# Kernel tuning notes

Measured on AMD Instinct MI355X. Metric: run time of the kernel, lower is better.

The kernel has to match this reference:

```python
import jax, jax.numpy as jnp
import numpy as np

N_WIRES = 4
N_REUP = 3
N_Q_LAYERS = 2
SEQ_LEN = 10
GRU_HIDDEN = 16


def setup_inputs() -> dict:
    key = jax.random.key(0)
    ks = jax.random.split(key, 24)
    N, E = 10000, 320000
    s = 0.25
    inp = {
        'x': jax.random.normal(ks[0], (N, SEQ_LEN + 3), jnp.float32),
        'edge_index': jax.random.randint(ks[1], (2, E), 0, N, dtype=jnp.int32),
        'edge_attr': jax.random.normal(ks[2], (E, 1), jnp.float32),
        'W_ih': jax.random.normal(ks[3], (3 * GRU_HIDDEN, 1), jnp.float32) * s,
        'W_hh': jax.random.normal(ks[4], (3 * GRU_HIDDEN, GRU_HIDDEN), jnp.float32) * s,
        'b_ih': jax.random.normal(ks[5], (3 * GRU_HIDDEN,), jnp.float32) * s,
        'b_hh': jax.random.normal(ks[6], (3 * GRU_HIDDEN,), jnp.float32) * s,
        'p1_W': jax.random.normal(ks[7], (N_WIRES, GRU_HIDDEN + 3), jnp.float32) * s,
        'p1_b': jax.random.normal(ks[8], (N_WIRES,), jnp.float32) * s,
        'a1_W': jax.random.normal(ks[9], (1, 2 * N_WIRES), jnp.float32) * s,
        'q1_w': jax.random.uniform(ks[10], (N_REUP, N_Q_LAYERS, 2), jnp.float32, -np.pi, np.pi),
        'g1': jnp.ones((N_WIRES,), jnp.float32),
        'be1': jnp.zeros((N_WIRES,), jnp.float32),
        'p2_W': jax.random.normal(ks[11], (N_WIRES, N_WIRES), jnp.float32) * s,
        'p2_b': jax.random.normal(ks[12], (N_WIRES,), jnp.float32) * s,
        'a2_W': jax.random.normal(ks[13], (1, 2 * N_WIRES), jnp.float32) * s,
        'q2_w': jax.random.uniform(ks[14], (N_REUP, N_Q_LAYERS, 2), jnp.float32, -np.pi, np.pi),
        'g2': jnp.ones((N_WIRES,), jnp.float32),
        'be2': jnp.zeros((N_WIRES,), jnp.float32),
        'r_W': jax.random.normal(ks[15], (1, N_WIRES), jnp.float32) * s,
        'r_b': jax.random.normal(ks[16], (1,), jnp.float32) * s,
    }
    return inp


def _ry(theta):
    c = jnp.cos(theta * 0.5)
    s = jnp.sin(theta * 0.5)
    return jnp.stack([jnp.stack([c, -s], -1), jnp.stack([s, c], -1)], -2).astype(jnp.complex64)


def _rz(theta):
    em = jnp.exp(-0.5j * theta)
    ep = jnp.exp(0.5j * theta)
    z = jnp.zeros_like(em)
    return jnp.stack([jnp.stack([em, z], -1), jnp.stack([z, ep], -1)], -2)


def _apply1q(state, gate, wire):
    # state: [E,2,2,2,2]; gate: [2,2] shared or [E,2,2] per-edge
    st = jnp.moveaxis(state, 1 + wire, -1)
    if gate.ndim == 3:
        st = jnp.einsum('eij,e...j->e...i', gate, st)
    else:
        st = jnp.einsum('ij,e...j->e...i', gate, st)
    return jnp.moveaxis(st, -1, 1 + wire)


def _cnot(state, c, t):
    st = jnp.moveaxis(state, (1 + c, 1 + t), (-2, -1))
    st = jnp.concatenate([st[..., :1, :], st[..., 1:, ::-1]], axis=-2)
    return jnp.moveaxis(st, (-2, -1), (1 + c, 1 + t))


def _qcircuit(inputs, corr, weights):
    # inputs: [E,4] angles, corr: [E], weights: [3,2,2]; batched 4-wire statevector sim
    E = inputs.shape[0]
    state = jnp.zeros((E, 16), jnp.complex64).at[:, 0].set(1.0).reshape(E, 2, 2, 2, 2)
    for r in range(N_REUP):
        for i in range(N_WIRES):
            state = _apply1q(state, _ry(inputs[:, i]), i)
        state = _apply1q(state, _ry(corr), 0)
        for d in range(N_Q_LAYERS):
            gy = _ry(weights[r, d, 0])
            gz = _rz(weights[r, d, 1])
            for i in range(N_WIRES):
                state = _apply1q(state, gy, i)
                state = _apply1q(state, gz, i)
            for i in range(d % 2, N_WIRES - 1, 2):
                state = _cnot(state, i, i + 1)
    probs = state.real ** 2 + state.imag ** 2
    z = jnp.array([1.0, -1.0], jnp.float32)
    return jnp.stack(
        [jnp.einsum('e...j,j->e', jnp.moveaxis(probs, 1 + w, -1), z) for w in range(N_WIRES)], -1)


def _layernorm(x, g, b):
    mu = x.mean(-1, keepdims=True)
    v = ((x - mu) ** 2).mean(-1, keepdims=True)
    return (x - mu) * jax.lax.rsqrt(v + 1e-5) * g + b


def _qgat(x, edge_index, edge_attr, Wp, bp, Wa, qw, g, b):
    N = x.shape[0]
    h = jax.nn.elu(x @ Wp.T + bp)  # [N,4]
    sl = jnp.arange(N, dtype=edge_index.dtype)
    src = jnp.concatenate([edge_index[0], sl])
    dst = jnp.concatenate([edge_index[1], sl])
    ea = jnp.concatenate([edge_attr[:, 0], jnp.ones((N,), x.dtype)])
    alpha = jnp.concatenate([h[src], h[dst]], -1) @ Wa[0]  # [Et]
    alpha = jax.nn.leaky_relu(alpha, 0.2) * jnp.abs(ea)
    alpha = alpha - jax.lax.stop_gradient(alpha).max()
    aexp = jnp.exp(alpha)
    dsum = jax.ops.segment_sum(aexp, dst, num_segments=N)
    alpha = aexp / (dsum[dst] + 1e-8)
    corr = jnp.tanh(ea) * jnp.pi
    msg = alpha[:, None] * _qcircuit(jnp.tanh(h[src]) * jnp.pi, corr, qw)  # [Et,4]
    aggr = jax.ops.segment_sum(msg, dst, num_segments=N)
    return _layernorm(aggr + h, g, b)


def _gru_last(price_seq, W_ih, W_hh, b_ih, b_hh):
    # price_seq: [N,T] scalar-per-step GRU; returns final hidden [N,H]
    N = price_seq.shape[0]
    h0 = jnp.zeros((N, GRU_HIDDEN), price_seq.dtype)
    w_in = W_ih[:, 0]  # [3H]

    def step(h, x_t):
        gi = x_t[:, None] * w_in + b_ih  # [N,3H]
        gh = h @ W_hh.T + b_hh
        ir, iz, inn = jnp.split(gi, 3, -1)
        hr, hz, hn = jnp.split(gh, 3, -1)
        r = jax.nn.sigmoid(ir + hr)
        z = jax.nn.sigmoid(iz + hz)
        n = jnp.tanh(inn + r * hn)
        return (1.0 - z) * n + z * h, None

    h, _ = jax.lax.scan(step, h0, price_seq.T)
    return h


def reference(x, edge_index, edge_attr, W_ih, W_hh, b_ih, b_hh,
              p1_W, p1_b, a1_W, q1_w, g1, be1,
              p2_W, p2_b, a2_W, q2_w, g2, be2, r_W, r_b):
    hT = _gru_last(x[:, :SEQ_LEN], W_ih, W_hh, b_ih, b_hh)
    h = jnp.concatenate([hT, x[:, SEQ_LEN:]], -1)  # [N,19]
    h = jax.nn.relu(_qgat(h, edge_index, edge_attr, p1_W, p1_b, a1_W, q1_w, g1, be1))
    h = _qgat(h, edge_index, edge_attr, p2_W, p2_b, a2_W, q2_w, g2, be2)
    return (h @ r_W.T + r_b)[:, 0]
```

## Files before the change

kernel.cpp:

```cpp
#include <hip/hip_runtime.h>
#include <math.h>


#define GH 16
#define SEQ 10
#define PI_F 3.14159265358979323846f

__device__ __forceinline__ float sigmoidf_(float x) { return 1.0f / (1.0f + expf(-x)); }

__global__ __launch_bounds__(256) void k_gru(
    const float* __restrict__ x, const float* __restrict__ W_ih,
    const float* __restrict__ W_hh, const float* __restrict__ b_ih,
    const float* __restrict__ b_hh, const float* __restrict__ p1W,
    const float* __restrict__ p1b, const float* __restrict__ a1W,
    const float* __restrict__ q1w, const float* __restrict__ q2w,
    const int* __restrict__ ei, int* __restrict__ deg,
    float* __restrict__ nrec1, float* __restrict__ hdd1,
    float* __restrict__ qcs, int N, int E)
{
    for (int e = blockIdx.x * 256 + threadIdx.x; e < E; e += gridDim.x * 256)
        atomicAdd(&deg[ei[E + e]], 1);

    __shared__ float sW[48 * 16];
    __shared__ float sp1W[4 * 19], sp1b[4];
    for (int i = threadIdx.x; i < 48 * 16; i += 256) sW[i] = W_hh[i];
    if (threadIdx.x < 76) sp1W[threadIdx.x] = p1W[threadIdx.x];
    if (threadIdx.x < 4) sp1b[threadIdx.x] = p1b[threadIdx.x];
    __syncthreads();

    if (blockIdx.x == 0 && threadIdx.x < 12) {
        const float* qw = (threadIdx.x < 6) ? q1w : q2w;
        int rd = threadIdx.x % 6;
        float sy, cy; sincosf(0.5f * qw[rd * 2 + 0], &sy, &cy);
        float sz, cz; sincosf(0.5f * qw[rd * 2 + 1], &sz, &cz);
        float* q = qcs + threadIdx.x * 4;
        q[0] = cy; q[1] = sy; q[2] = cz; q[3] = sz;
    }

    const int j = threadIdx.x & 15;
    const int n = blockIdx.x * 16 + (threadIdx.x >> 4);
    const bool valid = (n < N);

    float wr[GH], wz[GH], wn[GH];
#pragma unroll
    for (int k = 0; k < GH; ++k) {
        wr[k] = sW[j * 16 + k];
        wz[k] = sW[(16 + j) * 16 + k];
        wn[k] = sW[(32 + j) * 16 + k];
    }
    float wir = W_ih[j], wiz = W_ih[16 + j], win_ = W_ih[32 + j];
    float bir = b_ih[j], biz = b_ih[16 + j], bin_ = b_ih[32 + j];
    float brr = b_hh[j], brz = b_hh[16 + j], brn = b_hh[32 + j];

    float xv[13];
#pragma unroll
    for (int t = 0; t < 13; ++t) xv[t] = valid ? x[n * 13 + t] : 0.f;

    float h = 0.f;
#pragma unroll
    for (int t = 0; t < SEQ; ++t) {
        float xt = xv[t];
        float ghr = brr, ghz = brz, ghn = brn;
#pragma unroll
        for (int k = 0; k < GH; ++k) {
            float hk = __shfl(h, k, 16);
            ghr += wr[k] * hk; ghz += wz[k] * hk; ghn += wn[k] * hk;
        }
        float r  = sigmoidf_(xt * wir + bir + ghr);
        float z  = sigmoidf_(xt * wiz + biz + ghz);
        float nv = tanhf(xt * win_ + bin_ + r * ghn);
        h = (1.f - z) * nv + z * h;
    }

    float s0 = h * sp1W[0 * 19 + j];
    float s1 = h * sp1W[1 * 19 + j];
    float s2 = h * sp1W[2 * 19 + j];
    float s3 = h * sp1W[3 * 19 + j];
#pragma unroll
    for (int m = 1; m < 16; m <<= 1) {
        s0 += __shfl_xor(s0, m, 16);
        s1 += __shfl_xor(s1, m, 16);
        s2 += __shfl_xor(s2, m, 16);
        s3 += __shfl_xor(s3, m, 16);
    }
    if (valid && j < 4) {
        float s = (j == 0) ? s0 : (j == 1) ? s1 : (j == 2) ? s2 : s3;
        s += sp1b[j] + xv[10] * sp1W[j * 19 + 16] + xv[11] * sp1W[j * 19 + 17]
           + xv[12] * sp1W[j * 19 + 18];
        float hv = (s > 0.f) ? s : expm1f(s);
        float* nb = nrec1 + (size_t)n * 16;
        float sv, cv; sincosf(0.5f * PI_F * tanhf(hv), &sv, &cv);
        nb[2 * j]     = cv;
        nb[2 * j + 1] = sv;
        nb[12 + j]    = hv;
        float ds = hv * a1W[j];
        float dd = hv * a1W[4 + j];
        ds += __shfl_xor(ds, 1); ds += __shfl_xor(ds, 2);
        dd += __shfl_xor(dd, 1); dd += __shfl_xor(dd, 2);
        if (j == 0) { nb[8] = ds; hdd1[n] = dd; }
    }
}

__global__ __launch_bounds__(256) void k_scan(
    const int* __restrict__ deg, int* __restrict__ off,
    int* __restrict__ cur, int N)
{
    __shared__ int part[256];
    const int t = threadIdx.x;
    const int chunk = (N + 255) / 256;
    const int lo = t * chunk;
    const int hi = min(lo + chunk, N);
    int s = 0;
    for (int i = lo; i < hi; ++i) s += deg[i] + 1;
    part[t] = s;
    __syncthreads();
    for (int d = 1; d < 256; d <<= 1) {
        int y = (t >= d) ? part[t - d] : 0;
        __syncthreads();
        part[t] += y;
        __syncthreads();
    }
    int run = part[t] - s;
    for (int i = lo; i < hi; ++i) { off[i] = run; cur[i] = run; run += deg[i] + 1; }
}

__global__ __launch_bounds__(256) void k_fill(
    const int* __restrict__ ei, const float* __restrict__ ea,
    int* __restrict__ cur, float2* __restrict__ rec,
    int* __restrict__ dstv, int E, int N)
{
    int idx = blockIdx.x * 256 + threadIdx.x;
    if (idx >= E + N) return;
    int src, d; float ev;
    if (idx < E) { src = ei[idx]; d = ei[E + idx]; ev = ea[idx]; }
    else         { src = idx - E; d = src;         ev = 1.0f;    }
    int slot = atomicAdd(&cur[d], 1);
    float2 r; r.x = __int_as_float(src); r.y = ev;
    rec[slot] = r;
    dstv[slot] = d;
}

template <int STR>
__device__ __forceinline__ void ry_g(float (&sr)[16], float (&si)[16], float c, float s) {
#pragma unroll
    for (int i0 = 0; i0 < 16; ++i0) {
        if (i0 & STR) continue;
        int i1 = i0 | STR;
        float a0r = sr[i0], a0i = si[i0], a1r = sr[i1], a1i = si[i1];
        sr[i0] = c * a0r - s * a1r; si[i0] = c * a0i - s * a1i;
        sr[i1] = s * a0r + c * a1r; si[i1] = s * a0i + c * a1i;
    }
}
template <int STR>
__device__ __forceinline__ void rz_g(float (&sr)[16], float (&si)[16], float c, float s) {
#pragma unroll
    for (int i = 0; i < 16; ++i) {
        float r = sr[i], im = si[i];
        if (i & STR) { sr[i] = r * c - im * s; si[i] = im * c + r * s; }
        else         { sr[i] = r * c + im * s; si[i] = im * c - r * s; }
    }
}
template <int SC, int ST>
__device__ __forceinline__ void cnot_g(float (&sr)[16], float (&si)[16]) {
#pragma unroll
    for (int i = 0; i < 16; ++i) {
        if ((i & SC) && !(i & ST)) {
            int j = i | ST;
            float tr = sr[i], ti = si[i];
            sr[i] = sr[j]; si[i] = si[j]; sr[j] = tr; si[j] = ti;
        }
    }
}

__device__ __forceinline__ void qcirc(
    float mc, float ms, float c1, float s1, float c2, float s2,
    float c3, float s3, const float* __restrict__ qc, float (&z)[4])
{
    float sr[16], si[16];
    float t0 = mc * c1, t1 = mc * s1, t2 = ms * c1, t3 = ms * s1;
    float u0 = c2 * c3, u1 = c2 * s3, u2 = s2 * c3, u3 = s2 * s3;
    sr[0]  = t0 * u0; sr[1]  = t0 * u1; sr[2]  = t0 * u2; sr[3]  = t0 * u3;
    sr[4]  = t1 * u0; sr[5]  = t1 * u1; sr[6]  = t1 * u2; sr[7]  = t1 * u3;
    sr[8]  = t2 * u0; sr[9]  = t2 * u1; sr[10] = t2 * u2; sr[11] = t2 * u3;
    sr[12] = t3 * u0; sr[13] = t3 * u1; sr[14] = t3 * u2; sr[15] = t3 * u3;
#pragma unroll
    for (int i = 0; i < 16; ++i) si[i] = 0.f;

#pragma unroll
    for (int r = 0; r < 3; ++r) {
        if (r > 0) {
            ry_g<8>(sr, si, mc, ms);
            ry_g<4>(sr, si, c1, s1);
            ry_g<2>(sr, si, c2, s2);
            ry_g<1>(sr, si, c3, s3);
        }
#pragma unroll
        for (int d = 0; d < 2; ++d) {
            const bool lastd = (r == 2 && d == 1);
            int rd = r * 2 + d;
            float cy = qc[rd * 4 + 0], sy = qc[rd * 4 + 1];
            float cz = qc[rd * 4 + 2], sz = qc[rd * 4 + 3];
            ry_g<8>(sr, si, cy, sy); if (!lastd) rz_g<8>(sr, si, cz, sz);
            ry_g<4>(sr, si, cy, sy); if (!lastd) rz_g<4>(sr, si, cz, sz);
            ry_g<2>(sr, si, cy, sy); if (!lastd) rz_g<2>(sr, si, cz, sz);
            ry_g<1>(sr, si, cy, sy); if (!lastd) rz_g<1>(sr, si, cz, sz);
            if (d == 0) { cnot_g<8, 4>(sr, si); cnot_g<2, 1>(sr, si); }
            else        { cnot_g<4, 2>(sr, si); }
        }
    }

    float p[16];
#pragma unroll
    for (int i = 0; i < 16; ++i) p[i] = sr[i] * sr[i] + si[i] * si[i];
#pragma unroll
    for (int w = 0; w < 4; ++w) {
        const int STR = 8 >> w;
        float zz = 0.f;
#pragma unroll
        for (int i = 0; i < 16; ++i) if (!(i & STR)) zz += p[i];
        z[w] = 2.f * zz - 1.f;
    }
}

__global__ __launch_bounds__(256) void k_edge(
    const float2* __restrict__ rec, const int* __restrict__ dstv,
    const float* __restrict__ nrec, const float* __restrict__ hdd,
    const float* __restrict__ qcsL, float* __restrict__ S, int EN)
{
    const int slot = blockIdx.x * 256 + threadIdx.x;
    const int lane = threadIdx.x & 63;
    const bool valid = slot < EN;
    int dst = -1;
    float a0 = 0.f, a1 = 0.f, a2 = 0.f, a3 = 0.f, a4 = 0.f;

    if (valid) {
        dst = dstv[slot];
        float2 r = rec[slot];
        int src = __float_as_int(r.x);
        float eav = r.y;
        const float* sb = nrec + (size_t)src * 16;
        float4 c01 = *reinterpret_cast<const float4*>(sb);
        float4 c23 = *reinterpret_cast<const float4*>(sb + 4);
        float s0 = sb[8] + hdd[dst];
        s0 = (s0 > 0.f) ? s0 : 0.2f * s0;
        float aexp = expf(s0 * fabsf(eav));

        float scv, ccv; sincosf(0.5f * PI_F * tanhf(eav), &scv, &ccv);
        float mc = c01.x * ccv - c01.y * scv;
        float ms = c01.y * ccv + c01.x * scv;

        float z[4];
        qcirc(mc, ms, c01.z, c01.w, c23.x, c23.y, c23.z, c23.w, qcsL, z);
        a0 = aexp * z[0]; a1 = aexp * z[1]; a2 = aexp * z[2]; a3 = aexp * z[3];
        a4 = aexp;
    }

    int prevd = __shfl_up(dst, 1);
    bool head = (lane == 0) || (prevd != dst);
    unsigned long long hm = __ballot(head);
    unsigned long long below = (2ull << lane) - 1ull;
    int H = 63 - __clzll((long long)(hm & below));
    int dist = lane - H;
#pragma unroll
    for (int st = 1; st < 64; st <<= 1) {
        float t0 = __shfl_up(a0, st), t1 = __shfl_up(a1, st),
              t2 = __shfl_up(a2, st), t3 = __shfl_up(a3, st),
              t4 = __shfl_up(a4, st);
        if (dist >= st) { a0 += t0; a1 += t1; a2 += t2; a3 += t3; a4 += t4; }
    }
    int nextd = __shfl_down(dst, 1);
    bool lastl = (lane == 63) || (dst != nextd);
    if (lastl && dst >= 0) {
        float* sbase = S + (size_t)dst * 5;
        atomicAdd(sbase + 0, a0); atomicAdd(sbase + 1, a1);
        atomicAdd(sbase + 2, a2); atomicAdd(sbase + 3, a3);
        atomicAdd(sbase + 4, a4);
    }
}

template <bool FINAL>
__global__ __launch_bounds__(256) void k_node(
    const float* __restrict__ S, const float* __restrict__ nrec,
    const float* __restrict__ g4, const float* __restrict__ be4,
    const float* __restrict__ pW, const float* __restrict__ pb,
    const float* __restrict__ WaN, const float* __restrict__ rW,
    const float* __restrict__ rb, float* __restrict__ onrec,
    float* __restrict__ ohdd, float* __restrict__ out, int N)
{
    int n = blockIdx.x * 256 + threadIdx.x;
    if (n >= N) return;
    const float* sb = S + (size_t)n * 5;
    const float* nb = nrec + (size_t)n * 16;
    float dn = sb[4] + 1e-8f;
    float v0 = sb[0] / dn + nb[12];
    float v1 = sb[1] / dn + nb[13];
    float v2 = sb[2] / dn + nb[14];
    float v3 = sb[3] / dn + nb[15];
    float mu = 0.25f * (v0 + v1 + v2 + v3);
    float d0 = v0 - mu, d1 = v1 - mu, d2 = v2 - mu, d3 = v3 - mu;
    float var = 0.25f * (d0 * d0 + d1 * d1 + d2 * d2 + d3 * d3);
    float rs = 1.0f / sqrtf(var + 1e-5f);
    float y0 = d0 * rs * g4[0] + be4[0];
    float y1 = d1 * rs * g4[1] + be4[1];
    float y2 = d2 * rs * g4[2] + be4[2];
    float y3 = d3 * rs * g4[3] + be4[3];

    if (FINAL) {
        out[n] = rb[0] + y0 * rW[0] + y1 * rW[1] + y2 * rW[2] + y3 * rW[3];
    } else {
        y0 = fmaxf(y0, 0.f); y1 = fmaxf(y1, 0.f);
        y2 = fmaxf(y2, 0.f); y3 = fmaxf(y3, 0.f);
        float hv[4];
#pragma unroll
        for (int w = 0; w < 4; ++w) {
            float s = pb[w] + y0 * pW[w * 4 + 0] + y1 * pW[w * 4 + 1]
                    + y2 * pW[w * 4 + 2] + y3 * pW[w * 4 + 3];
            hv[w] = (s > 0.f) ? s : expm1f(s);
        }
        float* ob = onrec + (size_t)n * 16;
        float ds = 0.f, dd = 0.f;
#pragma unroll
        for (int w = 0; w < 4; ++w) {
            float sv, cv; sincosf(0.5f * PI_F * tanhf(hv[w]), &sv, &cv);
            ob[2 * w]     = cv;
            ob[2 * w + 1] = sv;
            ob[12 + w]    = hv[w];
            ds += hv[w] * WaN[w];
            dd += hv[w] * WaN[4 + w];
        }
        ob[8] = ds;
        ohdd[n] = dd;
    }
}

extern "C" void kernel_launch(void* const* d_in, const int* in_sizes, int n_in,
                              void* d_out, int out_size, void* d_ws, size_t ws_size,
                              hipStream_t stream)
{
    const float* x    = (const float*)d_in[0];
    const int*   ei   = (const int*)d_in[1];
    const float* ea   = (const float*)d_in[2];
    const float* W_ih = (const float*)d_in[3];
    const float* W_hh = (const float*)d_in[4];
    const float* b_ih = (const float*)d_in[5];
    const float* b_hh = (const float*)d_in[6];
    const float* p1W  = (const float*)d_in[7];
    const float* p1b  = (const float*)d_in[8];
    const float* a1W  = (const float*)d_in[9];
    const float* q1w  = (const float*)d_in[10];
    const float* g1   = (const float*)d_in[11];
    const float* be1  = (const float*)d_in[12];
    const float* p2W  = (const float*)d_in[13];
    const float* p2b  = (const float*)d_in[14];
    const float* a2W  = (const float*)d_in[15];
    const float* q2w  = (const float*)d_in[16];
    const float* g2   = (const float*)d_in[17];
    const float* be2  = (const float*)d_in[18];
    const float* rW   = (const float*)d_in[19];
    const float* rb   = (const float*)d_in[20];
    float* out = (float*)d_out;

    int N  = in_sizes[0] / 13;
    int E  = in_sizes[1] / 2;
    int EN = E + N;

    float* ws    = (float*)d_ws;
    float* nrec1 = ws;
    float* nrec2 = nrec1 + (size_t)N * 16;
    float* hdd1  = nrec2 + (size_t)N * 16;
    float* hdd2  = hdd1 + N;
    float* qcs   = hdd2 + N;
    float* S1    = qcs + 64;
    float* S2    = S1 + (size_t)N * 5;
    int* deg  = (int*)(S2 + (size_t)N * 5);
    int* off  = deg + N;
    int* cur  = off + N;
    int* dstv = cur + N;
    uintptr_t rp = (uintptr_t)(dstv + EN);
    rp = (rp + 15u) & ~(uintptr_t)15u;
    float2* rec = (float2*)rp;

    hipMemsetAsync(S1, 0, ((size_t)N * 10 + N) * sizeof(float), stream);

    const int B = 256;
    k_gru<<<(N + 15) / 16, B, 0, stream>>>(x, W_ih, W_hh, b_ih, b_hh, p1W, p1b,
                                           a1W, q1w, q2w, ei, deg, nrec1, hdd1,
                                           qcs, N, E);
    k_scan<<<1, B, 0, stream>>>(deg, off, cur, N);
    k_fill<<<(EN + B - 1) / B, B, 0, stream>>>(ei, ea, cur, rec, dstv, E, N);

    k_edge<<<(EN + B - 1) / B, B, 0, stream>>>(rec, dstv, nrec1, hdd1, qcs, S1, EN);
    k_node<false><<<(N + B - 1) / B, B, 0, stream>>>(
        S1, nrec1, g1, be1, p2W, p2b, a2W, rW, rb, nrec2, hdd2, out, N);

    k_edge<<<(EN + B - 1) / B, B, 0, stream>>>(rec, dstv, nrec2, hdd2, qcs + 24, S2, EN);
    k_node<true><<<(N + B - 1) / B, B, 0, stream>>>(
        S2, nrec2, g2, be2, p2W, p2b, a2W, rW, rb, nrec2, hdd2, out, N);
}
```

Before: 265.2 us.

## Precompute edge rotation in fill, process two edges per thread, widen scan

The fill kernel now computes the edge-attribute rotation (sincos of tanh) once and stores it with src and dst in a float4 record, plus |ea| in a separate array, so both edge passes skip that math. Each edge-kernel thread handles two slots (g and g+G), issuing all gathers up front to raise memory-level parallelism, and runs two segmented reductions. The scan runs with 1024 threads, and zeroing of the S buffers moves into the GRU kernel so only deg is memset. The cost is a larger per-edge record to read and more registers per thread in the edge kernel.

```diff
diff --git a/kernel.cpp b/kernel.cpp
--- a/kernel.cpp
+++ b/kernel.cpp
@@ -16,8 +16,10 @@
     const float* __restrict__ q1w, const float* __restrict__ q2w,
     const int* __restrict__ ei, int* __restrict__ deg,
     float* __restrict__ nrec1, float* __restrict__ hdd1,
-    float* __restrict__ qcs, int N, int E)
-{
+    float* __restrict__ qcs, float* __restrict__ Sz, int N, int E)
+{
+    for (int i = blockIdx.x * 256 + threadIdx.x; i < N * 10; i += gridDim.x * 256)
+        Sz[i] = 0.f;
     for (int e = blockIdx.x * 256 + threadIdx.x; e < E; e += gridDim.x * 256)
         atomicAdd(&deg[ei[E + e]], 1);
 
@@ -101,20 +103,20 @@
     }
 }
 
-__global__ __launch_bounds__(256) void k_scan(
+__global__ __launch_bounds__(1024) void k_scan(
     const int* __restrict__ deg, int* __restrict__ off,
     int* __restrict__ cur, int N)
 {
-    __shared__ int part[256];
+    __shared__ int part[1024];
     const int t = threadIdx.x;
-    const int chunk = (N + 255) / 256;
+    const int chunk = (N + 1023) / 1024;
     const int lo = t * chunk;
     const int hi = min(lo + chunk, N);
     int s = 0;
     for (int i = lo; i < hi; ++i) s += deg[i] + 1;
     part[t] = s;
     __syncthreads();
-    for (int d = 1; d < 256; d <<= 1) {
+    for (int d = 1; d < 1024; d <<= 1) {
         int y = (t >= d) ? part[t - d] : 0;
         __syncthreads();
         part[t] += y;
@@ -126,8 +128,8 @@
 
 __global__ __launch_bounds__(256) void k_fill(
     const int* __restrict__ ei, const float* __restrict__ ea,
-    int* __restrict__ cur, float2* __restrict__ rec,
-    int* __restrict__ dstv, int E, int N)
+    int* __restrict__ cur, float4* __restrict__ rec,
+    float* __restrict__ aeav, int E, int N)
 {
     int idx = blockIdx.x * 256 + threadIdx.x;
     if (idx >= E + N) return;
@@ -135,9 +137,12 @@
     if (idx < E) { src = ei[idx]; d = ei[E + idx]; ev = ea[idx]; }
     else         { src = idx - E; d = src;         ev = 1.0f;    }
     int slot = atomicAdd(&cur[d], 1);
-    float2 r; r.x = __int_as_float(src); r.y = ev;
+    float scv, ccv; sincosf(0.5f * PI_F * tanhf(ev), &scv, &ccv);
+    float4 r;
+    r.x = __int_as_float(src); r.y = __int_as_float(d);
+    r.z = ccv; r.w = scv;
     rec[slot] = r;
-    dstv[slot] = d;
+    aeav[slot] = fabsf(ev);
 }
 
 template <int STR>
@@ -222,39 +227,10 @@
     }
 }
 
-__global__ __launch_bounds__(256) void k_edge(
-    const float2* __restrict__ rec, const int* __restrict__ dstv,
-    const float* __restrict__ nrec, const float* __restrict__ hdd,
-    const float* __restrict__ qcsL, float* __restrict__ S, int EN)
-{
-    const int slot = blockIdx.x * 256 + threadIdx.x;
-    const int lane = threadIdx.x & 63;
-    const bool valid = slot < EN;
-    int dst = -1;
-    float a0 = 0.f, a1 = 0.f, a2 = 0.f, a3 = 0.f, a4 = 0.f;
-
-    if (valid) {
-        dst = dstv[slot];
-        float2 r = rec[slot];
-        int src = __float_as_int(r.x);
-        float eav = r.y;
-        const float* sb = nrec + (size_t)src * 16;
-        float4 c01 = *reinterpret_cast<const float4*>(sb);
-        float4 c23 = *reinterpret_cast<const float4*>(sb + 4);
-        float s0 = sb[8] + hdd[dst];
-        s0 = (s0 > 0.f) ? s0 : 0.2f * s0;
-        float aexp = expf(s0 * fabsf(eav));
-
-        float scv, ccv; sincosf(0.5f * PI_F * tanhf(eav), &scv, &ccv);
-        float mc = c01.x * ccv - c01.y * scv;
-        float ms = c01.y * ccv + c01.x * scv;
-
-        float z[4];
-        qcirc(mc, ms, c01.z, c01.w, c23.x, c23.y, c23.z, c23.w, qcsL, z);
-        a0 = aexp * z[0]; a1 = aexp * z[1]; a2 = aexp * z[2]; a3 = aexp * z[3];
-        a4 = aexp;
-    }
-
+__device__ __forceinline__ void segreduce(
+    int dst, int lane, float a0, float a1, float a2, float a3, float a4,
+    float* __restrict__ S)
+{
     int prevd = __shfl_up(dst, 1);
     bool head = (lane == 0) || (prevd != dst);
     unsigned long long hm = __ballot(head);
@@ -276,6 +252,62 @@
         atomicAdd(sbase + 2, a2); atomicAdd(sbase + 3, a3);
         atomicAdd(sbase + 4, a4);
     }
+}
+
+__global__ __launch_bounds__(256) void k_edge(
+    const float4* __restrict__ rec, const float* __restrict__ aeav,
+    const float* __restrict__ nrec, const float* __restrict__ hdd,
+    const float* __restrict__ qcsL, float* __restrict__ S, int EN, int G)
+{
+    const int g = blockIdx.x * 256 + threadIdx.x;
+    const int lane = threadIdx.x & 63;
+    const int sA = g, sB = g + G;
+    const bool vA = sA < EN, vB = sB < EN;
+
+    float4 rA = vA ? rec[sA] : make_float4(0.f, 0.f, 1.f, 0.f);
+    float4 rB = vB ? rec[sB] : make_float4(0.f, 0.f, 1.f, 0.f);
+    float aeA = vA ? aeav[sA] : 0.f;
+    float aeB = vB ? aeav[sB] : 0.f;
+    int srcA = __float_as_int(rA.x), dstA = vA ? __float_as_int(rA.y) : -1;
+    int srcB = __float_as_int(rB.x), dstB = vB ? __float_as_int(rB.y) : -1;
+    const float* sbA = nrec + (size_t)(vA ? srcA : 0) * 16;
+    const float* sbB = nrec + (size_t)(vB ? srcB : 0) * 16;
+    float4 c01A = *reinterpret_cast<const float4*>(sbA);
+    float4 c23A = *reinterpret_cast<const float4*>(sbA + 4);
+    float hsA = sbA[8];
+    float hdA = hdd[vA ? dstA : 0];
+    float4 c01B = *reinterpret_cast<const float4*>(sbB);
+    float4 c23B = *reinterpret_cast<const float4*>(sbB + 4);
+    float hsB = sbB[8];
+    float hdB = hdd[vB ? dstB : 0];
+
+    float a0 = 0.f, a1 = 0.f, a2 = 0.f, a3 = 0.f, a4 = 0.f;
+    if (vA) {
+        float s0 = hsA + hdA;
+        s0 = (s0 > 0.f) ? s0 : 0.2f * s0;
+        float aexp = expf(s0 * aeA);
+        float mc = c01A.x * rA.z - c01A.y * rA.w;
+        float ms = c01A.y * rA.z + c01A.x * rA.w;
+        float z[4];
+        qcirc(mc, ms, c01A.z, c01A.w, c23A.x, c23A.y, c23A.z, c23A.w, qcsL, z);
+        a0 = aexp * z[0]; a1 = aexp * z[1]; a2 = aexp * z[2]; a3 = aexp * z[3];
+        a4 = aexp;
+    }
+    segreduce(dstA, lane, a0, a1, a2, a3, a4, S);
+
+    a0 = a1 = a2 = a3 = a4 = 0.f;
+    if (vB) {
+        float s0 = hsB + hdB;
+        s0 = (s0 > 0.f) ? s0 : 0.2f * s0;
+        float aexp = expf(s0 * aeB);
+        float mc = c01B.x * rB.z - c01B.y * rB.w;
+        float ms = c01B.y * rB.z + c01B.x * rB.w;
+        float z[4];
+        qcirc(mc, ms, c01B.z, c01B.w, c23B.x, c23B.y, c23B.z, c23B.w, qcsL, z);
+        a0 = aexp * z[0]; a1 = aexp * z[1]; a2 = aexp * z[2]; a3 = aexp * z[3];
+        a4 = aexp;
+    }
+    segreduce(dstB, lane, a0, a1, a2, a3, a4, S);
 }
 
 template <bool FINAL>
@@ -372,28 +404,32 @@
     float* qcs   = hdd2 + N;
     float* S1    = qcs + 64;
     float* S2    = S1 + (size_t)N * 5;
-    int* deg  = (int*)(S2 + (size_t)N * 5);
+    float* aeav  = S2 + (size_t)N * 5;
+    int* deg  = (int*)(aeav + EN);
     int* off  = deg + N;
     int* cur  = off + N;
-    int* dstv = cur + N;
-    uintptr_t rp = (uintptr_t)(dstv + EN);
+    uintptr_t rp = (uintptr_t)(cur + N);
     rp = (rp + 15u) & ~(uintptr_t)15u;
-    float2* rec = (float2*)rp;
-
-    hipMemsetAsync(S1, 0, ((size_t)N * 10 + N) * sizeof(float), stream);
+    float4* rec = (float4*)rp;
+
+    hipMemsetAsync(deg, 0, (size_t)N * sizeof(int), stream);
 
     const int B = 256;
     k_gru<<<(N + 15) / 16, B, 0, stream>>>(x, W_ih, W_hh, b_ih, b_hh, p1W, p1b,
                                            a1W, q1w, q2w, ei, deg, nrec1, hdd1,
-                                           qcs, N, E);
-    k_scan<<<1, B, 0, stream>>>(deg, off, cur, N);
-    k_fill<<<(EN + B - 1) / B, B, 0, stream>>>(ei, ea, cur, rec, dstv, E, N);
-
-    k_edge<<<(EN + B - 1) / B, B, 0, stream>>>(rec, dstv, nrec1, hdd1, qcs, S1, EN);
+                                           qcs, S1, N, E);
+    k_scan<<<1, 1024, 0, stream>>>(deg, off, cur, N);
+    k_fill<<<(EN + B - 1) / B, B, 0, stream>>>(ei, ea, cur, rec, aeav, E, N);
+
+    int half = (EN + 1) / 2;
+    int eblocks = (half + B - 1) / B;
+    int G = eblocks * B;
+
+    k_edge<<<eblocks, B, 0, stream>>>(rec, aeav, nrec1, hdd1, qcs, S1, EN, G);
     k_node<false><<<(N + B - 1) / B, B, 0, stream>>>(
         S1, nrec1, g1, be1, p2W, p2b, a2W, rW, rb, nrec2, hdd2, out, N);
 
-    k_edge<<<(EN + B - 1) / B, B, 0, stream>>>(rec, dstv, nrec2, hdd2, qcs + 24, S2, EN);
+    k_edge<<<eblocks, B, 0, stream>>>(rec, aeav, nrec2, hdd2, qcs + 24, S2, EN, G);
     k_node<true><<<(N + B - 1) / B, B, 0, stream>>>(
         S2, nrec2, g2, be2, p2W, p2b, a2W, rW, rb, nrec2, hdd2, out, N);
 }
```

Result: faster. 257.2 us (-3.0%).

## Precompute per-node quantum circuit moments so edge kernel evaluates a quadratic form

Applied to the files above, without the earlier changes.

The circuit's dependence on the edge is isolated to wire 0's rotation, so the per-node part of the circuit (fixed gate matrices plus the node's encoding) is folded into a per-node table of 40 quadratic coefficients. The edge kernel then only needs a degree-6 polynomial in cos/sin rather than simulating the 16-amplitude state for every edge. Edge-attribute trig is moved into the CSR fill, src/dst are packed into one word, the S zeroing moves into the GRU kernel, and the scan uses 1024 threads. The packing assumes node ids fit in 16 bits, and the per-node table adds an extra kernel and 48 floats of traffic per node.

```diff
diff --git a/kernel.cpp b/kernel.cpp
--- a/kernel.cpp
+++ b/kernel.cpp
@@ -13,11 +13,12 @@
     const float* __restrict__ W_hh, const float* __restrict__ b_ih,
     const float* __restrict__ b_hh, const float* __restrict__ p1W,
     const float* __restrict__ p1b, const float* __restrict__ a1W,
-    const float* __restrict__ q1w, const float* __restrict__ q2w,
     const int* __restrict__ ei, int* __restrict__ deg,
     float* __restrict__ nrec1, float* __restrict__ hdd1,
-    float* __restrict__ qcs, int N, int E)
-{
+    float* __restrict__ Sz, int N, int E)
+{
+    for (int i = blockIdx.x * 256 + threadIdx.x; i < N * 10; i += gridDim.x * 256)
+        Sz[i] = 0.f;
     for (int e = blockIdx.x * 256 + threadIdx.x; e < E; e += gridDim.x * 256)
         atomicAdd(&deg[ei[E + e]], 1);
 
@@ -27,15 +28,6 @@
     if (threadIdx.x < 76) sp1W[threadIdx.x] = p1W[threadIdx.x];
     if (threadIdx.x < 4) sp1b[threadIdx.x] = p1b[threadIdx.x];
     __syncthreads();
-
-    if (blockIdx.x == 0 && threadIdx.x < 12) {
-        const float* qw = (threadIdx.x < 6) ? q1w : q2w;
-        int rd = threadIdx.x % 6;
-        float sy, cy; sincosf(0.5f * qw[rd * 2 + 0], &sy, &cy);
-        float sz, cz; sincosf(0.5f * qw[rd * 2 + 1], &sz, &cz);
-        float* q = qcs + threadIdx.x * 4;
-        q[0] = cy; q[1] = sy; q[2] = cz; q[3] = sz;
-    }
 
     const int j = threadIdx.x & 15;
     const int n = blockIdx.x * 16 + (threadIdx.x >> 4);
@@ -101,20 +93,20 @@
     }
 }
 
-__global__ __launch_bounds__(256) void k_scan(
+__global__ __launch_bounds__(1024) void k_scan(
     const int* __restrict__ deg, int* __restrict__ off,
     int* __restrict__ cur, int N)
 {
-    __shared__ int part[256];
+    __shared__ int part[1024];
     const int t = threadIdx.x;
-    const int chunk = (N + 255) / 256;
+    const int chunk = (N + 1023) / 1024;
     const int lo = t * chunk;
     const int hi = min(lo + chunk, N);
     int s = 0;
     for (int i = lo; i < hi; ++i) s += deg[i] + 1;
     part[t] = s;
     __syncthreads();
-    for (int d = 1; d < 256; d <<= 1) {
+    for (int d = 1; d < 1024; d <<= 1) {
         int y = (t >= d) ? part[t - d] : 0;
         __syncthreads();
         part[t] += y;
@@ -126,8 +118,7 @@
 
 __global__ __launch_bounds__(256) void k_fill(
     const int* __restrict__ ei, const float* __restrict__ ea,
-    int* __restrict__ cur, float2* __restrict__ rec,
-    int* __restrict__ dstv, int E, int N)
+    int* __restrict__ cur, float4* __restrict__ rec, int E, int N)
 {
     int idx = blockIdx.x * 256 + threadIdx.x;
     if (idx >= E + N) return;
@@ -135,9 +126,12 @@
     if (idx < E) { src = ei[idx]; d = ei[E + idx]; ev = ea[idx]; }
     else         { src = idx - E; d = src;         ev = 1.0f;    }
     int slot = atomicAdd(&cur[d], 1);
-    float2 r; r.x = __int_as_float(src); r.y = ev;
+    float scv, ccv; sincosf(0.5f * PI_F * tanhf(ev), &scv, &ccv);
+    float4 r;
+    r.x = __int_as_float(src | (d << 16));
+    r.y = fabsf(ev);
+    r.z = ccv; r.w = scv;
     rec[slot] = r;
-    dstv[slot] = d;
 }
 
 template <int STR>
@@ -172,89 +166,161 @@
     }
 }
 
-__device__ __forceinline__ void qcirc(
-    float mc, float ms, float c1, float s1, float c2, float s2,
-    float c3, float s3, const float* __restrict__ qc, float (&z)[4])
-{
+__global__ __launch_bounds__(128) void k_gmat(
+    const float* __restrict__ q1w, const float* __restrict__ q2w,
+    float* __restrict__ Gtab)
+{
+    int t = threadIdx.x;
+    if (t >= 96) return;
+    int layer = t / 48, rem = t % 48, rep = rem / 16, col = rem % 16;
+    const float* qw = layer ? q2w : q1w;
     float sr[16], si[16];
-    float t0 = mc * c1, t1 = mc * s1, t2 = ms * c1, t3 = ms * s1;
-    float u0 = c2 * c3, u1 = c2 * s3, u2 = s2 * c3, u3 = s2 * s3;
-    sr[0]  = t0 * u0; sr[1]  = t0 * u1; sr[2]  = t0 * u2; sr[3]  = t0 * u3;
-    sr[4]  = t1 * u0; sr[5]  = t1 * u1; sr[6]  = t1 * u2; sr[7]  = t1 * u3;
-    sr[8]  = t2 * u0; sr[9]  = t2 * u1; sr[10] = t2 * u2; sr[11] = t2 * u3;
-    sr[12] = t3 * u0; sr[13] = t3 * u1; sr[14] = t3 * u2; sr[15] = t3 * u3;
-#pragma unroll
-    for (int i = 0; i < 16; ++i) si[i] = 0.f;
-
-#pragma unroll
-    for (int r = 0; r < 3; ++r) {
-        if (r > 0) {
-            ry_g<8>(sr, si, mc, ms);
-            ry_g<4>(sr, si, c1, s1);
-            ry_g<2>(sr, si, c2, s2);
-            ry_g<1>(sr, si, c3, s3);
-        }
-#pragma unroll
-        for (int d = 0; d < 2; ++d) {
-            const bool lastd = (r == 2 && d == 1);
-            int rd = r * 2 + d;
-            float cy = qc[rd * 4 + 0], sy = qc[rd * 4 + 1];
-            float cz = qc[rd * 4 + 2], sz = qc[rd * 4 + 3];
-            ry_g<8>(sr, si, cy, sy); if (!lastd) rz_g<8>(sr, si, cz, sz);
-            ry_g<4>(sr, si, cy, sy); if (!lastd) rz_g<4>(sr, si, cz, sz);
-            ry_g<2>(sr, si, cy, sy); if (!lastd) rz_g<2>(sr, si, cz, sz);
-            ry_g<1>(sr, si, cy, sy); if (!lastd) rz_g<1>(sr, si, cz, sz);
-            if (d == 0) { cnot_g<8, 4>(sr, si); cnot_g<2, 1>(sr, si); }
-            else        { cnot_g<4, 2>(sr, si); }
-        }
-    }
-
-    float p[16];
-#pragma unroll
-    for (int i = 0; i < 16; ++i) p[i] = sr[i] * sr[i] + si[i] * si[i];
-#pragma unroll
-    for (int w = 0; w < 4; ++w) {
-        const int STR = 8 >> w;
-        float zz = 0.f;
-#pragma unroll
-        for (int i = 0; i < 16; ++i) if (!(i & STR)) zz += p[i];
-        z[w] = 2.f * zz - 1.f;
-    }
-}
-
-__global__ __launch_bounds__(256) void k_edge(
-    const float2* __restrict__ rec, const int* __restrict__ dstv,
-    const float* __restrict__ nrec, const float* __restrict__ hdd,
-    const float* __restrict__ qcsL, float* __restrict__ S, int EN)
-{
-    const int slot = blockIdx.x * 256 + threadIdx.x;
-    const int lane = threadIdx.x & 63;
-    const bool valid = slot < EN;
-    int dst = -1;
-    float a0 = 0.f, a1 = 0.f, a2 = 0.f, a3 = 0.f, a4 = 0.f;
-
-    if (valid) {
-        dst = dstv[slot];
-        float2 r = rec[slot];
-        int src = __float_as_int(r.x);
-        float eav = r.y;
-        const float* sb = nrec + (size_t)src * 16;
-        float4 c01 = *reinterpret_cast<const float4*>(sb);
-        float4 c23 = *reinterpret_cast<const float4*>(sb + 4);
-        float s0 = sb[8] + hdd[dst];
-        s0 = (s0 > 0.f) ? s0 : 0.2f * s0;
-        float aexp = expf(s0 * fabsf(eav));
-
-        float scv, ccv; sincosf(0.5f * PI_F * tanhf(eav), &scv, &ccv);
-        float mc = c01.x * ccv - c01.y * scv;
-        float ms = c01.y * ccv + c01.x * scv;
-
-        float z[4];
-        qcirc(mc, ms, c01.z, c01.w, c23.x, c23.y, c23.z, c23.w, qcsL, z);
-        a0 = aexp * z[0]; a1 = aexp * z[1]; a2 = aexp * z[2]; a3 = aexp * z[3];
-        a4 = aexp;
-    }
-
+#pragma unroll
+    for (int i = 0; i < 16; ++i) { sr[i] = 0.f; si[i] = 0.f; }
+    sr[col] = 1.f;
+#pragma unroll
+    for (int d = 0; d < 2; ++d) {
+        float cy, sy, cz, sz;
+        sincosf(0.5f * qw[(rep * 2 + d) * 2 + 0], &sy, &cy);
+        sincosf(0.5f * qw[(rep * 2 + d) * 2 + 1], &sz, &cz);
+        bool lastd = (rep == 2) && (d == 1);
+        ry_g<8>(sr, si, cy, sy); if (!lastd) rz_g<8>(sr, si, cz, sz);
+        ry_g<4>(sr, si, cy, sy); if (!lastd) rz_g<4>(sr, si, cz, sz);
+        ry_g<2>(sr, si, cy, sy); if (!lastd) rz_g<2>(sr, si, cz, sz);
+        ry_g<1>(sr, si, cy, sy); if (!lastd) rz_g<1>(sr, si, cz, sz);
+        if (d == 0) { cnot_g<8, 4>(sr, si); cnot_g<2, 1>(sr, si); }
+        else        { cnot_g<4, 2>(sr, si); }
+    }
+    float* g = Gtab + layer * 1536 + rep * 512;
+#pragma unroll
+    for (int i = 0; i < 16; ++i) {
+        g[(i * 16 + col) * 2 + 0] = sr[i];
+        g[(i * 16 + col) * 2 + 1] = si[i];
+    }
+}
+
+__global__ __launch_bounds__(256) void k_prep(
+    const float* __restrict__ nrec, const float* __restrict__ Gl,
+    float* __restrict__ T, int N)
+{
+    __shared__ float gr[3][16 * 17], gi[3][16 * 17];
+    for (int idx = threadIdx.x; idx < 3 * 256; idx += 256) {
+        int rep = idx >> 8, rc = idx & 255, i = rc >> 4, jj = rc & 15;
+        gr[rep][i * 17 + jj] = Gl[rep * 512 + rc * 2 + 0];
+        gi[rep][i * 17 + jj] = Gl[rep * 512 + rc * 2 + 1];
+    }
+    __syncthreads();
+
+    const int lane = threadIdx.x & 15;
+    const int n = blockIdx.x * 16 + (threadIdx.x >> 4);
+    if (n >= N) return;
+    const float* nb = nrec + (size_t)n * 16;
+    const float c1 = nb[2], s1 = nb[3], c2 = nb[4], s2 = nb[5], c3 = nb[6], s3 = nb[7];
+
+    float pa = (lane & 8) ? 0.f
+             : ((lane & 4) ? s1 : c1) * ((lane & 2) ? s2 : c2) * ((lane & 1) ? s3 : c3);
+    float pb;
+    { float t = __shfl_xor(pa, 8, 16); pb = (lane & 8) ? t : -t; }
+
+    float ar = 0.f, ai = 0.f, br = 0.f, bi = 0.f;
+#pragma unroll
+    for (int jj = 0; jj < 16; ++jj) {
+        float Gr = gr[0][lane * 17 + jj], Gi = gi[0][lane * 17 + jj];
+        float xa = __shfl(pa, jj, 16), xb = __shfl(pb, jj, 16);
+        ar += Gr * xa; ai += Gi * xa; br += Gr * xb; bi += Gi * xb;
+    }
+
+#define BFLY(vr, vi, STR, cc, ss) { \
+    float tr_ = __shfl_xor(vr, STR, 16), ti_ = __shfl_xor(vi, STR, 16); \
+    float sg_ = (lane & STR) ? (ss) : -(ss); \
+    vr = (cc) * vr + sg_ * tr_; vi = (cc) * vi + sg_ * ti_; }
+#define R123(vr, vi) { BFLY(vr, vi, 4, c1, s1) BFLY(vr, vi, 2, c2, s2) BFLY(vr, vi, 1, c3, s3) }
+#define KAPP(orr, oii, xr, xi) { \
+    float tr_ = __shfl_xor(xr, 8, 16), ti_ = __shfl_xor(xi, 8, 16); \
+    orr = (lane & 8) ? tr_ : -tr_; oii = (lane & 8) ? ti_ : -ti_; }
+
+    R123(ar, ai) R123(br, bi)
+
+    float sr4[4], si4[4];
+    sr4[0] = ar; si4[0] = ai;
+    KAPP(sr4[1], si4[1], ar, ai)
+    sr4[2] = br; si4[2] = bi;
+    KAPP(sr4[3], si4[3], br, bi)
+
+    float nr4[4] = {0.f, 0.f, 0.f, 0.f}, ni4[4] = {0.f, 0.f, 0.f, 0.f};
+#pragma unroll
+    for (int jj = 0; jj < 16; ++jj) {
+        float Gr = gr[1][lane * 17 + jj], Gi = gi[1][lane * 17 + jj];
+#pragma unroll
+        for (int v = 0; v < 4; ++v) {
+            float xr = __shfl(sr4[v], jj, 16), xi = __shfl(si4[v], jj, 16);
+            nr4[v] += Gr * xr - Gi * xi;
+            ni4[v] += Gr * xi + Gi * xr;
+        }
+    }
+#pragma unroll
+    for (int v = 0; v < 4; ++v) { R123(nr4[v], ni4[v]) }
+
+    float gr4[4], gi4[4];
+    float m01r = nr4[1] + nr4[2], m01i = ni4[1] + ni4[2];
+    gr4[0] = nr4[0]; gi4[0] = ni4[0];
+    { float kr, ki; KAPP(kr, ki, nr4[0], ni4[0]) gr4[1] = m01r + kr; gi4[1] = m01i + ki; }
+    { float kr, ki; KAPP(kr, ki, m01r, m01i)     gr4[2] = nr4[3] + kr; gi4[2] = ni4[3] + ki; }
+    { float kr, ki; KAPP(kr, ki, nr4[3], ni4[3]) gr4[3] = kr; gi4[3] = ki; }
+
+    float vr4[4] = {0.f, 0.f, 0.f, 0.f}, vi4[4] = {0.f, 0.f, 0.f, 0.f};
+#pragma unroll
+    for (int jj = 0; jj < 16; ++jj) {
+        float Gr = gr[2][lane * 17 + jj], Gi = gi[2][lane * 17 + jj];
+#pragma unroll
+        for (int v = 0; v < 4; ++v) {
+            float xr = __shfl(gr4[v], jj, 16), xi = __shfl(gi4[v], jj, 16);
+            vr4[v] += Gr * xr - Gi * xi;
+            vi4[v] += Gr * xi + Gi * xr;
+        }
+    }
+
+    float p[10];
+    {
+        int idx = 0;
+#pragma unroll
+        for (int k = 0; k < 4; ++k)
+#pragma unroll
+            for (int l = 0; l < 4; ++l) {
+                if (l < k) continue;
+                p[idx++] = vr4[k] * vr4[l] + vi4[k] * vi4[l];
+            }
+    }
+#pragma unroll
+    for (int pi = 0; pi < 10; ++pi) {
+        float v = p[pi];
+#pragma unroll
+        for (int m = 8; m >= 1; m >>= 1) {
+            float t = __shfl_xor(v, m, 16);
+            v = (lane & m) ? (t - v) : (v + t);
+        }
+        p[pi] = v;
+    }
+
+    float* Tb = T + (size_t)n * 48;
+    int w = (lane == 8) ? 0 : (lane == 4) ? 1 : (lane == 2) ? 2 : (lane == 1) ? 3 : -1;
+    if (w >= 0) {
+#pragma unroll
+        for (int pi = 0; pi < 10; ++pi) {
+            float mult = (pi == 0 || pi == 4 || pi == 7 || pi == 9) ? 1.f : 2.f;
+            Tb[w * 10 + pi] = mult * p[pi];
+        }
+    }
+    if (lane == 0) { Tb[40] = nb[0]; Tb[41] = nb[1]; Tb[42] = nb[8]; Tb[43] = 0.f; }
+#undef BFLY
+#undef R123
+#undef KAPP
+}
+
+__device__ __forceinline__ void segreduce(
+    int dst, int lane, float a0, float a1, float a2, float a3, float a4,
+    float* __restrict__ S)
+{
     int prevd = __shfl_up(dst, 1);
     bool head = (lane == 0) || (prevd != dst);
     unsigned long long hm = __ballot(head);
@@ -276,6 +342,59 @@
         atomicAdd(sbase + 2, a2); atomicAdd(sbase + 3, a3);
         atomicAdd(sbase + 4, a4);
     }
+}
+
+__global__ __launch_bounds__(256) void k_edge(
+    const float4* __restrict__ rec, const float* __restrict__ T,
+    const float* __restrict__ hdd, float* __restrict__ S, int EN)
+{
+    const int slot = blockIdx.x * 256 + threadIdx.x;
+    const int lane = threadIdx.x & 63;
+    int dst = -1;
+    float acc0 = 0.f, acc1 = 0.f, acc2 = 0.f, acc3 = 0.f, acc4 = 0.f;
+
+    if (slot < EN) {
+        float4 r = rec[slot];
+        int ids = __float_as_int(r.x);
+        int src = ids & 0xFFFF;
+        dst = ids >> 16;
+        float aea = r.y, ccv = r.z, scv = r.w;
+
+        const float* Tb = T + (size_t)src * 48;
+        float t[44];
+#pragma unroll
+        for (int q = 0; q < 11; ++q) {
+            float4 v4 = *reinterpret_cast<const float4*>(Tb + q * 4);
+            t[q * 4 + 0] = v4.x; t[q * 4 + 1] = v4.y;
+            t[q * 4 + 2] = v4.z; t[q * 4 + 3] = v4.w;
+        }
+        float hdN = hdd[dst];
+
+        float mc = t[40] * ccv - t[41] * scv;
+        float ms = t[41] * ccv + t[40] * scv;
+        float m2 = mc * mc, s2 = ms * ms;
+        float cf0 = mc * m2, cf1 = m2 * ms, cf2 = mc * s2, cf3 = ms * s2;
+        float qq[10];
+        qq[0] = cf0 * cf0; qq[1] = cf0 * cf1; qq[2] = cf0 * cf2; qq[3] = cf0 * cf3;
+        qq[4] = cf1 * cf1; qq[5] = cf1 * cf2; qq[6] = cf1 * cf3;
+        qq[7] = cf2 * cf2; qq[8] = cf2 * cf3; qq[9] = cf3 * cf3;
+
+        float z0 = 0.f, z1 = 0.f, z2 = 0.f, z3 = 0.f;
+#pragma unroll
+        for (int pi = 0; pi < 10; ++pi) {
+            z0 += t[pi] * qq[pi];
+            z1 += t[10 + pi] * qq[pi];
+            z2 += t[20 + pi] * qq[pi];
+            z3 += t[30 + pi] * qq[pi];
+        }
+
+        float s0a = t[42] + hdN;
+        s0a = (s0a > 0.f) ? s0a : 0.2f * s0a;
+        float aexp = expf(s0a * aea);
+        acc0 = aexp * z0; acc1 = aexp * z1; acc2 = aexp * z2; acc3 = aexp * z3;
+        acc4 = aexp;
+    }
+    segreduce(dst, lane, acc0, acc1, acc2, acc3, acc4, S);
 }
 
 template <bool FINAL>
@@ -369,31 +488,33 @@
     float* nrec2 = nrec1 + (size_t)N * 16;
     float* hdd1  = nrec2 + (size_t)N * 16;
     float* hdd2  = hdd1 + N;
-    float* qcs   = hdd2 + N;
-    float* S1    = qcs + 64;
+    float* S1    = hdd2 + N;
     float* S2    = S1 + (size_t)N * 5;
-    int* deg  = (int*)(S2 + (size_t)N * 5);
+    float* Gtab  = S2 + (size_t)N * 5;
+    float* T     = Gtab + 3072;
+    int* deg  = (int*)(T + (size_t)N * 48);
     int* off  = deg + N;
     int* cur  = off + N;
-    int* dstv = cur + N;
-    uintptr_t rp = (uintptr_t)(dstv + EN);
+    uintptr_t rp = (uintptr_t)(cur + N);
     rp = (rp + 15u) & ~(uintptr_t)15u;
-    float2* rec = (float2*)rp;
-
-    hipMemsetAsync(S1, 0, ((size_t)N * 10 + N) * sizeof(float), stream);
+    float4* rec = (float4*)rp;
+
+    hipMemsetAsync(deg, 0, (size_t)N * sizeof(int), stream);
 
     const int B = 256;
     k_gru<<<(N + 15) / 16, B, 0, stream>>>(x, W_ih, W_hh, b_ih, b_hh, p1W, p1b,
-                                           a1W, q1w, q2w, ei, deg, nrec1, hdd1,
-                                           qcs, N, E);
-    k_scan<<<1, B, 0, stream>>>(deg, off, cur, N);
-    k_fill<<<(EN + B - 1) / B, B, 0, stream>>>(ei, ea, cur, rec, dstv, E, N);
-
-    k_edge<<<(EN + B - 1) / B, B, 0, stream>>>(rec, dstv, nrec1, hdd1, qcs, S1, EN);
+                                           a1W, ei, deg, nrec1, hdd1, S1, N, E);
+    k_scan<<<1, 1024, 0, stream>>>(deg, off, cur, N);
+    k_fill<<<(EN + B - 1) / B, B, 0, stream>>>(ei, ea, cur, rec, E, N);
+    k_gmat<<<1, 128, 0, stream>>>(q1w, q2w, Gtab);
+
+    k_prep<<<(N + 15) / 16, B, 0, stream>>>(nrec1, Gtab, T, N);
+    k_edge<<<(EN + B - 1) / B, B, 0, stream>>>(rec, T, hdd1, S1, EN);
     k_node<false><<<(N + B - 1) / B, B, 0, stream>>>(
         S1, nrec1, g1, be1, p2W, p2b, a2W, rW, rb, nrec2, hdd2, out, N);
 
-    k_edge<<<(EN + B - 1) / B, B, 0, stream>>>(rec, dstv, nrec2, hdd2, qcs + 24, S2, EN);
+    k_prep<<<(N + 15) / 16, B, 0, stream>>>(nrec2, Gtab + 1536, T, N);
+    k_edge<<<(EN + B - 1) / B, B, 0, stream>>>(rec, T, hdd2, S2, EN);
     k_node<true><<<(N + B - 1) / B, B, 0, stream>>>(
         S2, nrec2, g2, be2, p2W, p2b, a2W, rW, rb, nrec2, hdd2, out, N);
 }
```

Measured after the change: 238.3 us. -10.1%, faster.
